# Optimization experiments

Measured on AMD Instinct MI355X. Metric: run time of the kernel, lower is better.

## Reference

```python
import jax, jax.numpy as jnp
import numpy as np

B, C, HD, NL, NP = 2, 256, 8, 4, 4
D = C // HD
SHAPES = np.array([[128, 128], [64, 64], [32, 32], [16, 16]], dtype=np.int64)
LV = int(SHAPES.prod(axis=1).sum())  # 21760
LQ = LV


def _bilinear(v_l, loc, Hl, Wl):
    # v_l: [B, HD, Nl, D]; loc: [B, Q, HD, P, 2] normalized to [0,1]
    # Matches torch grid_sample(bilinear, padding='zeros', align_corners=False)
    Bq, Q, _, P, _ = loc.shape
    x = loc[..., 0] * Wl - 0.5
    y = loc[..., 1] * Hl - 0.5
    x0f = jnp.floor(x)
    y0f = jnp.floor(y)
    lx, ly = x - x0f, y - y0f
    x0 = x0f.astype(jnp.int32)
    y0 = y0f.astype(jnp.int32)

    def corner(xi, yi, w):
        valid = (xi >= 0) & (xi < Wl) & (yi >= 0) & (yi < Hl)
        idx = jnp.clip(yi, 0, Hl - 1) * Wl + jnp.clip(xi, 0, Wl - 1)  # [B,Q,HD,P]
        idx = idx.transpose(0, 2, 1, 3).reshape(Bq, HD, Q * P)
        g = jnp.take_along_axis(v_l, idx[..., None], axis=2).reshape(Bq, HD, Q, P, D)
        wm = jnp.where(valid, w, 0.0).transpose(0, 2, 1, 3)[..., None]  # [B,HD,Q,P,1]
        return g * wm

    return (corner(x0, y0, (1 - lx) * (1 - ly))
            + corner(x0 + 1, y0, lx * (1 - ly))
            + corner(x0, y0 + 1, (1 - lx) * ly)
            + corner(x0 + 1, y0 + 1, lx * ly))


def _msda(query, reference_points, value, shapes, W_off, b_off, W_attn, b_attn, W_val, b_val, W_out, b_out):
    # value projection -> per-head layout [B, HD, Lv, D]
    v = (value @ W_val + b_val).reshape(B, LV, HD, D).transpose(0, 2, 1, 3)
    off = (query @ W_off + b_off).reshape(B, LQ, HD, NL, NP, 2)
    aw = jax.nn.softmax((query @ W_attn + b_attn).reshape(B, LQ, HD, NL * NP), axis=-1)
    aw = aw.reshape(B, LQ, HD, NL, NP)
    norm = jnp.asarray(shapes[:, ::-1].copy(), query.dtype)  # (W_l, H_l) per level
    # sampling locations: [B, Lq, HD, NL, NP, 2]
    loc = reference_points[:, :, None, :, None, :] + off / norm[None, None, None, :, None, :]
    out = jnp.zeros((B, HD, LQ, D), query.dtype)
    start = 0
    for l in range(NL):  # small static loop over feature levels
        Hl, Wl = int(shapes[l, 0]), int(shapes[l, 1])
        samp = _bilinear(v[:, :, start:start + Hl * Wl], loc[:, :, :, l], Hl, Wl)  # [B,HD,Q,P,D]
        out = out + jnp.einsum('bhqpd,bhqp->bhqd', samp, aw[:, :, :, l].transpose(0, 2, 1, 3))
        start += Hl * Wl
    out = out.transpose(0, 2, 1, 3).reshape(B, LQ, C)
    # output projection + residual (identity = query, dropout inactive at eval)
    return out @ W_out + b_out + query


def setup_inputs():
    key = jax.random.key(0)
    ks = jax.random.split(key, 8)
    sc = 1.0 / np.sqrt(C)
    return {
        "query": jax.random.normal(ks[0], (B, LQ, C), jnp.float32),
        "reference_points": jax.random.uniform(ks[1], (B, LQ, NL, 2), dtype=jnp.float32),
        "value": jax.random.normal(ks[2], (B, LV, C), jnp.float32),
        "spatial_shapes": SHAPES,
        "level_start_index": np.concatenate([[0], np.cumsum(SHAPES.prod(axis=1))[:-1]]).astype(np.int64),
        "W_off": jax.random.normal(ks[3], (C, HD * NL * NP * 2), jnp.float32) * 0.01,
        "b_off": jax.random.normal(ks[4], (HD * NL * NP * 2,), jnp.float32) * 0.01,
        "W_attn": jax.random.normal(ks[5], (C, HD * NL * NP), jnp.float32) * 0.02,
        "b_attn": jnp.zeros((HD * NL * NP,), jnp.float32),
        "W_val": jax.random.normal(ks[6], (C, C), jnp.float32) * sc,
        "b_val": jnp.zeros((C,), jnp.float32),
        "W_out": jax.random.normal(ks[7], (C, C), jnp.float32) * sc,
        "b_out": jnp.zeros((C,), jnp.float32),
    }


def reference(query, reference_points, value, spatial_shapes, level_start_index, W_off, b_off, W_attn, b_attn, W_val, b_val, W_out, b_out):
    shapes = np.asarray(spatial_shapes)  # static level geometry
    del level_start_index  # level offsets derived directly from shapes
    return _msda(query, reference_points, value, shapes, W_off, b_off, W_attn, b_attn, W_val, b_val, W_out, b_out)
```

## Files before the change

### kernel.cpp

```cpp
#include <hip/hip_runtime.h>

#define LQN 21760
#define LVN 21760
#define BATCH 2
#define CDIM 256
#define HDN 8
#define DDIM 32
#define PADCELLS 22736

typedef __attribute__((ext_vector_type(8))) short short8;
typedef __attribute__((ext_vector_type(4))) float f32x4;
typedef __attribute__((ext_vector_type(2))) float f32x2;

__device__ __forceinline__ unsigned short f2bf(float f) {
  union { float f; unsigned int u; } v; v.f = f;
  unsigned int r = v.u + 0x7fffu + ((v.u >> 16) & 1u);
  return (unsigned short)(r >> 16);
}
__device__ __forceinline__ float bflo(unsigned int u) {
  union { unsigned int u; float f; } v; v.u = u << 16; return v.f;
}
__device__ __forceinline__ float bfhi(unsigned int u) {
  union { unsigned int u; float f; } v; v.u = u & 0xffff0000u; return v.f;
}
__device__ __forceinline__ unsigned pk2bf(float lo, float hi) {
  unsigned r;
  asm("v_cvt_pk_bf16_f32 %0, %1, %2" : "=v"(r) : "v"(lo), "v"(hi));
  return r;
}

template <int IMM>
__device__ __forceinline__ float swzf(float v) {
  return __int_as_float(__builtin_amdgcn_ds_swizzle(__float_as_int(v), IMM));
}
template <int IMM>
__device__ __forceinline__ unsigned swzu(unsigned v) {
  return (unsigned)__builtin_amdgcn_ds_swizzle((int)v, IMM);
}

__global__ __launch_bounds__(256) void zero_border_kernel(
    unsigned short* __restrict__ vbf) {
  const int img = blockIdx.y;
  const int tid = blockIdx.x * 256 + threadIdx.x;
  const int cell = tid >> 2;
  const int chunk = tid & 3;
  if (cell >= 976) return;
  const int lvl = (cell >= 516) + (cell >= 776) + (cell >= 908);
  const int base = (lvl == 0) ? 0 : (lvl == 1) ? 516 : (lvl == 2) ? 776 : 908;
  const int W2 = (lvl == 0) ? 130 : (lvl == 1) ? 66 : (lvl == 2) ? 34 : 18;
  const int pst = (lvl == 0) ? 0 : (lvl == 1) ? 16900 : (lvl == 2) ? 21256 : 22412;
  const int b = cell - base;
  int x, y;
  if (b < W2) { y = 0; x = b; }
  else if (b < 2 * W2) { y = W2 - 1; x = b - W2; }
  else { const int r = b - 2 * W2; y = 1 + (r >> 1); x = (r & 1) ? (W2 - 1) : 0; }
  const size_t off = (((size_t)img * PADCELLS + pst + y * W2 + x) << 5) + chunk * 8;
  *(uint4*)(vbf + off) = (uint4){0u, 0u, 0u, 0u};
}

__global__ __launch_bounds__(256) void prep_kernel(
    const float* __restrict__ Wval, const float* __restrict__ Woff,
    const float* __restrict__ Wattn, const float* __restrict__ Wout,
    unsigned short* __restrict__ wtval, unsigned short* __restrict__ wtoa,
    unsigned short* __restrict__ wtout) {
  int idx = blockIdx.x * 256 + threadIdx.x;
  int n = idx >> 8, k = idx & 255;
  if (idx < 65536) {
    wtval[idx] = f2bf(Wval[k * 256 + n]);
    wtout[idx] = f2bf(Wout[k * 256 + n]);
  }
  if (idx < 98304) {
    float v = (n < 256) ? Woff[k * 256 + n] : Wattn[k * 128 + (n - 256)];
    wtoa[idx] = f2bf(v);
  }
}

template <int MODE>
__global__ __launch_bounds__(256) void gemm_kernel(
    const float* __restrict__ Af32, const unsigned short* __restrict__ Abf,
    const unsigned short* __restrict__ Wt, const float* __restrict__ bias0,
    const float* __restrict__ bias1, const float* __restrict__ resid,
    unsigned short* __restrict__ out_bf, float* __restrict__ out_f32) {
  constexpr int K = 256;
  constexpr int LDSS = 40;
  __shared__ unsigned short lsA[2][128 * LDSS];
  __shared__ unsigned short lsB[2][128 * LDSS];
  const int m0 = blockIdx.x * 128;
  const int n0 = blockIdx.y * 128;
  const int t = threadIdx.x;
  const int w = t >> 6;
  const int l = t & 63;
  const int wr = (w >> 1) * 64;
  const int wc = (w & 1) * 64;
  const int fr = l & 15;
  const int kk = (l >> 4) * 8;

  f32x4 acc[4][4];
#pragma unroll
  for (int mi = 0; mi < 4; ++mi)
#pragma unroll
    for (int ci = 0; ci < 4; ++ci) acc[mi][ci] = (f32x4){0.f, 0.f, 0.f, 0.f};

  const int srow = t >> 1;
  const int sk = (t & 1) * 16;

  float4 fa[4];
  uint4 ua2[2];
  uint4 ub[2];

#define LOADA(kt)                                                           \
  do {                                                                      \
    const int k0_ = (kt) * 32;                                              \
    if (MODE == 2) {                                                        \
      const unsigned short* ap = Abf + (size_t)(m0 + srow) * K + k0_ + sk;  \
      ua2[0] = *(const uint4*)ap;                                           \
      ua2[1] = *(const uint4*)(ap + 8);                                     \
    } else {                                                                \
      const float* ap = Af32 + (size_t)(m0 + srow) * K + k0_ + sk;          \
      fa[0] = *(const float4*)(ap);                                         \
      fa[1] = *(const float4*)(ap + 4);                                     \
      fa[2] = *(const float4*)(ap + 8);                                     \
      fa[3] = *(const float4*)(ap + 12);                                    \
    }                                                                       \
    const unsigned short* bp = Wt + (size_t)(n0 + srow) * K + k0_ + sk;     \
    ub[0] = *(const uint4*)bp;                                              \
    ub[1] = *(const uint4*)(bp + 8);                                        \
  } while (0)

#define STOREL(buf)                                                         \
  do {                                                                      \
    unsigned short* la = &lsA[buf][0];                                      \
    unsigned short* lb = &lsB[buf][0];                                      \
    if (MODE == 2) {                                                        \
      *(uint4*)(la + srow * LDSS + sk) = ua2[0];                            \
      *(uint4*)(la + srow * LDSS + sk + 8) = ua2[1];                        \
    } else {                                                                \
      uint4 p0, p1;                                                         \
      p0.x = pk2bf(fa[0].x, fa[0].y);                                       \
      p0.y = pk2bf(fa[0].z, fa[0].w);                                       \
      p0.z = pk2bf(fa[1].x, fa[1].y);                                       \
      p0.w = pk2bf(fa[1].z, fa[1].w);                                       \
      p1.x = pk2bf(fa[2].x, fa[2].y);                                       \
      p1.y = pk2bf(fa[2].z, fa[2].w);                                       \
      p1.z = pk2bf(fa[3].x, fa[3].y);                                       \
      p1.w = pk2bf(fa[3].z, fa[3].w);                                       \
      *(uint4*)(la + srow * LDSS + sk) = p0;                                \
      *(uint4*)(la + srow * LDSS + sk + 8) = p1;                            \
    }                                                                       \
    *(uint4*)(lb + srow * LDSS + sk) = ub[0];                               \
    *(uint4*)(lb + srow * LDSS + sk + 8) = ub[1];                           \
  } while (0)

  LOADA(0);
  STOREL(0);
  __syncthreads();

#pragma unroll
  for (int kt = 0; kt < 8; ++kt) {
    if (kt < 7) LOADA(kt + 1);
    const unsigned short* la = &lsA[kt & 1][0];
    const unsigned short* lb = &lsB[kt & 1][0];
    short8 af[4], bfr[4];
#pragma unroll
    for (int mi = 0; mi < 4; ++mi)
      af[mi] = *(const short8*)(la + (wr + mi * 16 + fr) * LDSS + kk);
#pragma unroll
    for (int ci = 0; ci < 4; ++ci)
      bfr[ci] = *(const short8*)(lb + (wc + ci * 16 + fr) * LDSS + kk);
#pragma unroll
    for (int mi = 0; mi < 4; ++mi)
#pragma unroll
      for (int ci = 0; ci < 4; ++ci)
        acc[mi][ci] = __builtin_amdgcn_mfma_f32_16x16x32_bf16(
            af[mi], bfr[ci], acc[mi][ci], 0, 0, 0);
    if (kt < 7) STOREL((kt + 1) & 1);
    __syncthreads();
  }
#undef LOADA
#undef STOREL

  const int fq = l >> 4;
  if (MODE == 0) {
    int rbase[16];
#pragma unroll
    for (int mi = 0; mi < 4; ++mi) {
#pragma unroll
      for (int r = 0; r < 4; ++r) {
        const int row = m0 + wr + mi * 16 + fq * 4 + r;
        const int bb = (row >= LVN) ? 1 : 0;
        const int i = row - bb * LVN;
        const int lvl = (i >= 16384) + (i >= 20480) + (i >= 21504);
        const int stl = (lvl == 0) ? 0 : (lvl == 1) ? 16384 : (lvl == 2) ? 20480 : 21504;
        const int pst = (lvl == 0) ? 0 : (lvl == 1) ? 16900 : (lvl == 2) ? 21256 : 22412;
        const int lw = 7 - lvl;
        const int Wl = 128 >> lvl;
        const int loc = i - stl;
        const int y = loc >> lw;
        const int x = loc & (Wl - 1);
        const int pidx = pst + (y + 1) * (Wl + 2) + (x + 1);
        rbase[mi * 4 + r] = bb * (HDN * PADCELLS * DDIM) + pidx * DDIM;
      }
    }
#pragma unroll
    for (int ci = 0; ci < 4; ++ci) {
      const int col = n0 + wc + ci * 16 + fr;
      const float bias = bias0[col];
      const int cterm = (col >> 5) * (PADCELLS * DDIM) + (col & 31);
#pragma unroll
      for (int mi = 0; mi < 4; ++mi) {
#pragma unroll
        for (int r = 0; r < 4; r += 2) {
          const unsigned u =
              pk2bf(acc[mi][ci][r] + bias, acc[mi][ci][r + 1] + bias);
          out_bf[(size_t)(rbase[mi * 4 + r] + cterm)] = (unsigned short)u;
          out_bf[(size_t)(rbase[mi * 4 + r + 1] + cterm)] =
              (unsigned short)(u >> 16);
        }
      }
    }
  } else if (MODE == 1) {
#pragma unroll
    for (int ci = 0; ci < 4; ++ci) {
      const int col = n0 + wc + ci * 16 + fr;
      const float bias = (col < 256) ? bias0[col] : bias1[col - 256];
#pragma unroll
      for (int mi = 0; mi < 4; ++mi) {
        const int row0 = m0 + wr + mi * 16 + fq * 4;
#pragma unroll
        for (int r = 0; r < 4; r += 2) {
          const unsigned u =
              pk2bf(acc[mi][ci][r] + bias, acc[mi][ci][r + 1] + bias);
          out_bf[(size_t)(row0 + r) * 384 + col] = (unsigned short)u;
          out_bf[(size_t)(row0 + r + 1) * 384 + col] = (unsigned short)(u >> 16);
        }
      }
    }
  } else {
#pragma unroll
    for (int ci = 0; ci < 4; ++ci) {
      const int col = n0 + wc + ci * 16 + fr;
      const float bias = bias0[col];
#pragma unroll
      for (int mi = 0; mi < 4; ++mi) {
#pragma unroll
        for (int r = 0; r < 4; ++r) {
          const int row = m0 + wr + mi * 16 + fq * 4 + r;
          const size_t o = (size_t)row * 256 + col;
          out_f32[o] = acc[mi][ci][r] + bias + resid[o];
        }
      }
    }
  }
}

__global__ __launch_bounds__(256) void sampler_kernel(
    const unsigned short* __restrict__ vbf,
    const unsigned short* __restrict__ offattn,
    const float* __restrict__ refpts,
    unsigned short* __restrict__ msout) {
  const int lid = blockIdx.x;
  const int pair = lid & 7;
  const int k = lid >> 3;
  const int img = pair * 2 + (k & 1);
  const int qchunk = k >> 1;
  const int h = img & 7;
  const int bb = img >> 3;

  const int t = threadIdx.x;
  const int lane = t & 63;
  const int qloc = qchunk * 64 + (t >> 6) * 16 + (lane >> 2);
  const int qi = bb * LQN + qloc;
  const int j = lane & 3;
  const int d0 = j * 8;

  const unsigned short* oa = offattn + (size_t)qi * 384;

  const int Wl = 128 >> j;
  const int W2 = Wl + 2;
  const int pst = (j == 0) ? 0 : (j == 1) ? 16900 : (j == 2) ? 21256 : 22412;
  const float fw = (float)Wl;

  const uint2 lr = *(const uint2*)(oa + 256 + h * 16 + j * 4);
  const float l0 = bflo(lr.x), l1 = bfhi(lr.x);
  const float l2 = bflo(lr.y), l3 = bfhi(lr.y);
  float mx = fmaxf(fmaxf(l0, l1), fmaxf(l2, l3));
  mx = fmaxf(mx, swzf<0x041F>(mx));
  mx = fmaxf(mx, swzf<0x081F>(mx));
  const float e0v = __expf(l0 - mx), e1v = __expf(l1 - mx);
  const float e2v = __expf(l2 - mx), e3v = __expf(l3 - mx);
  float s = (e0v + e1v) + (e2v + e3v);
  s += swzf<0x041F>(s);
  s += swzf<0x081F>(s);
  const float inv = 1.f / s;
  const float aw4[4] = {e0v * inv, e1v * inv, e2v * inv, e3v * inv};

  const float2 rf = *(const float2*)(refpts + (size_t)qi * 8 + j * 2);
  const uint4 ov = *(const uint4*)(oa + h * 32 + j * 8);
  const unsigned op_[4] = {ov.x, ov.y, ov.z, ov.w};

  unsigned eo[4][4];
  float wt[4][4];
#pragma unroll
  for (int pt = 0; pt < 4; ++pt) {
    const float ox = bflo(op_[pt]);
    const float oy = bfhi(op_[pt]);
    const float xs = fmaf(rf.x, fw, ox) - 0.5f;
    const float ys = fmaf(rf.y, fw, oy) - 0.5f;
    const float x0f = floorf(xs), y0f = floorf(ys);
    const float lx = xs - x0f, ly = ys - y0f;
    const int x0 = (int)x0f, y0 = (int)y0f;
    const float a = aw4[pt];
    const float wy1 = a * ly, wy0 = a - wy1;
    const float w01v = wy0 * lx, w00v = wy0 - w01v;
    const float w11v = wy1 * lx, w10v = wy1 - w11v;
    const int xb0 = min(max(x0 + 1, 0), Wl + 1);
    const int xb1 = min(max(x0 + 2, 0), Wl + 1);
    const int yb0 = min(max(y0 + 1, 0), Wl + 1);
    const int yb1 = min(max(y0 + 2, 0), Wl + 1);
    const unsigned r0 = (unsigned)(pst + yb0 * W2);
    const unsigned r1 = (unsigned)(pst + yb1 * W2);
    eo[pt][0] = (r0 + xb0) << 5;
    eo[pt][1] = (r0 + xb1) << 5;
    eo[pt][2] = (r1 + xb0) << 5;
    eo[pt][3] = (r1 + xb1) << 5;
    wt[pt][0] = w00v; wt[pt][1] = w01v; wt[pt][2] = w10v; wt[pt][3] = w11v;
  }

  const unsigned headbase =
      (unsigned)img * (PADCELLS * DDIM) + (unsigned)d0;

  f32x2 acc0 = (f32x2){0.f, 0.f}, acc1 = (f32x2){0.f, 0.f};
  f32x2 acc2 = (f32x2){0.f, 0.f}, acc3 = (f32x2){0.f, 0.f};

#define ACCUM(rv, wgt)                                 \
  {                                                    \
    f32x2 v_;                                          \
    v_.x = bflo(rv.x); v_.y = bfhi(rv.x);              \
    acc0 += v_ * (wgt);                                \
    v_.x = bflo(rv.y); v_.y = bfhi(rv.y);              \
    acc1 += v_ * (wgt);                                \
    v_.x = bflo(rv.z); v_.y = bfhi(rv.z);              \
    acc2 += v_ * (wgt);                                \
    v_.x = bflo(rv.w); v_.y = bfhi(rv.w);              \
    acc3 += v_ * (wgt);                                \
  }

#define POINT(LVL, PT)                                                  \
  {                                                                     \
    constexpr int IMM = (LVL << 5) | 0x1C;                              \
    const unsigned o00 = swzu<IMM>(eo[PT][0]);                          \
    const unsigned o01 = swzu<IMM>(eo[PT][1]);                          \
    const unsigned o10 = swzu<IMM>(eo[PT][2]);                          \
    const unsigned o11 = swzu<IMM>(eo[PT][3]);                          \
    const float w00 = swzf<IMM>(wt[PT][0]);                             \
    const float w01 = swzf<IMM>(wt[PT][1]);                             \
    const float w10 = swzf<IMM>(wt[PT][2]);                             \
    const float w11 = swzf<IMM>(wt[PT][3]);                             \
    const uint4 v00 = *(const uint4*)(vbf + headbase + o00);            \
    const uint4 v01 = *(const uint4*)(vbf + headbase + o01);            \
    const uint4 v10 = *(const uint4*)(vbf + headbase + o10);            \
    const uint4 v11 = *(const uint4*)(vbf + headbase + o11);            \
    ACCUM(v00, w00)                                                     \
    ACCUM(v01, w01)                                                     \
    ACCUM(v10, w10)                                                     \
    ACCUM(v11, w11)                                                     \
  }

  POINT(0, 0) POINT(0, 1) POINT(0, 2) POINT(0, 3)
  POINT(1, 0) POINT(1, 1) POINT(1, 2) POINT(1, 3)
  POINT(2, 0) POINT(2, 1) POINT(2, 2) POINT(2, 3)
  POINT(3, 0) POINT(3, 1) POINT(3, 2) POINT(3, 3)
#undef POINT
#undef ACCUM

  uint4 outv;
  outv.x = pk2bf(acc0.x, acc0.y);
  outv.y = pk2bf(acc1.x, acc1.y);
  outv.z = pk2bf(acc2.x, acc2.y);
  outv.w = pk2bf(acc3.x, acc3.y);
  *(uint4*)(msout + (size_t)qi * 256 + h * 32 + d0) = outv;
}

extern "C" void kernel_launch(void* const* d_in, const int* in_sizes, int n_in,
                              void* d_out, int out_size, void* d_ws,
                              size_t ws_size, hipStream_t stream) {
  const float* query = (const float*)d_in[0];
  const float* refpts = (const float*)d_in[1];
  const float* value = (const float*)d_in[2];
  const float* W_off = (const float*)d_in[5];
  const float* b_off = (const float*)d_in[6];
  const float* W_attn = (const float*)d_in[7];
  const float* b_attn = (const float*)d_in[8];
  const float* W_val = (const float*)d_in[9];
  const float* b_val = (const float*)d_in[10];
  const float* W_out = (const float*)d_in[11];
  const float* b_out = (const float*)d_in[12];
  float* out = (float*)d_out;

  char* ws = (char*)d_ws;
  unsigned short* wtval = (unsigned short*)(ws);
  unsigned short* wtoa = (unsigned short*)(ws + 131072);
  unsigned short* wtout = (unsigned short*)(ws + 327680);
  unsigned short* vbf = (unsigned short*)(ws + 458752);
  unsigned short* offattn = (unsigned short*)(ws + 23740416);
  unsigned short* msout = (unsigned short*)(ws + 57163776);

  zero_border_kernel<<<dim3(16, 16), 256, 0, stream>>>(vbf);
  prep_kernel<<<384, 256, 0, stream>>>(W_val, W_off, W_attn, W_out, wtval, wtoa,
                                       wtout);
  gemm_kernel<0><<<dim3(340, 2), 256, 0, stream>>>(
      value, nullptr, wtval, b_val, nullptr, nullptr, vbf, nullptr);
  gemm_kernel<1><<<dim3(340, 3), 256, 0, stream>>>(
      query, nullptr, wtoa, b_off, b_attn, nullptr, offattn, nullptr);
  sampler_kernel<<<5440, 256, 0, stream>>>(vbf, offattn, refpts, msout);
  gemm_kernel<2><<<dim3(340, 2), 256, 0, stream>>>(
      nullptr, msout, wtout, b_out, nullptr, query, nullptr, out);
}
```

Baseline: 176.2 us.

## Merge prep/zero kernels and value/offset GEMMs into fewer launches, coalesce GEMM loads

Folds the border-zeroing kernel into the weight-prep kernel and runs the value and offset/attention projection GEMMs as one interleaved 1700-block launch, cutting two launches and letting both GEMMs share the GPU. The GEMM tile loaders now have consecutive threads read consecutive 16-byte chunks across more rows instead of two wide chunks per row, which is meant to improve global-load coalescing and LDS store patterns. The merged GEMM kernel has a runtime branch on block ID, which may add some register pressure.

```diff
diff --git a/kernel.cpp b/kernel.cpp
--- a/kernel.cpp
+++ b/kernel.cpp
@@ -38,55 +38,54 @@
   return (unsigned)__builtin_amdgcn_ds_swizzle((int)v, IMM);
 }
 
-__global__ __launch_bounds__(256) void zero_border_kernel(
-    unsigned short* __restrict__ vbf) {
-  const int img = blockIdx.y;
-  const int tid = blockIdx.x * 256 + threadIdx.x;
-  const int cell = tid >> 2;
-  const int chunk = tid & 3;
-  if (cell >= 976) return;
-  const int lvl = (cell >= 516) + (cell >= 776) + (cell >= 908);
-  const int base = (lvl == 0) ? 0 : (lvl == 1) ? 516 : (lvl == 2) ? 776 : 908;
-  const int W2 = (lvl == 0) ? 130 : (lvl == 1) ? 66 : (lvl == 2) ? 34 : 18;
-  const int pst = (lvl == 0) ? 0 : (lvl == 1) ? 16900 : (lvl == 2) ? 21256 : 22412;
-  const int b = cell - base;
-  int x, y;
-  if (b < W2) { y = 0; x = b; }
-  else if (b < 2 * W2) { y = W2 - 1; x = b - W2; }
-  else { const int r = b - 2 * W2; y = 1 + (r >> 1); x = (r & 1) ? (W2 - 1) : 0; }
-  const size_t off = (((size_t)img * PADCELLS + pst + y * W2 + x) << 5) + chunk * 8;
-  *(uint4*)(vbf + off) = (uint4){0u, 0u, 0u, 0u};
-}
-
-__global__ __launch_bounds__(256) void prep_kernel(
+__global__ __launch_bounds__(256) void prep_zero_kernel(
     const float* __restrict__ Wval, const float* __restrict__ Woff,
     const float* __restrict__ Wattn, const float* __restrict__ Wout,
     unsigned short* __restrict__ wtval, unsigned short* __restrict__ wtoa,
-    unsigned short* __restrict__ wtout) {
-  int idx = blockIdx.x * 256 + threadIdx.x;
-  int n = idx >> 8, k = idx & 255;
-  if (idx < 65536) {
-    wtval[idx] = f2bf(Wval[k * 256 + n]);
-    wtout[idx] = f2bf(Wout[k * 256 + n]);
-  }
-  if (idx < 98304) {
-    float v = (n < 256) ? Woff[k * 256 + n] : Wattn[k * 128 + (n - 256)];
+    unsigned short* __restrict__ wtout, unsigned short* __restrict__ vbf) {
+  const int b = blockIdx.x;
+  if (b < 384) {
+    const int idx = b * 256 + threadIdx.x;
+    const int n = idx >> 8, k = idx & 255;
+    if (idx < 65536) {
+      wtval[idx] = f2bf(Wval[k * 256 + n]);
+      wtout[idx] = f2bf(Wout[k * 256 + n]);
+    }
+    const float v = (n < 256) ? Woff[k * 256 + n] : Wattn[k * 128 + (n - 256)];
     wtoa[idx] = f2bf(v);
+  } else {
+    const int b2 = b - 384;
+    const int img = b2 >> 4;
+    const int tid = (b2 & 15) * 256 + threadIdx.x;
+    const int cell = tid >> 2;
+    const int chunk = tid & 3;
+    if (cell >= 976) return;
+    const int lvl = (cell >= 516) + (cell >= 776) + (cell >= 908);
+    const int base = (lvl == 0) ? 0 : (lvl == 1) ? 516 : (lvl == 2) ? 776 : 908;
+    const int W2 = (lvl == 0) ? 130 : (lvl == 1) ? 66 : (lvl == 2) ? 34 : 18;
+    const int pst = (lvl == 0) ? 0 : (lvl == 1) ? 16900 : (lvl == 2) ? 21256 : 22412;
+    const int bb = cell - base;
+    int x, y;
+    if (bb < W2) { y = 0; x = bb; }
+    else if (bb < 2 * W2) { y = W2 - 1; x = bb - W2; }
+    else { const int r = bb - 2 * W2; y = 1 + (r >> 1); x = (r & 1) ? (W2 - 1) : 0; }
+    const size_t off = (((size_t)img * PADCELLS + pst + y * W2 + x) << 5) + chunk * 8;
+    *(uint4*)(vbf + off) = (uint4){0u, 0u, 0u, 0u};
   }
 }
 
 template <int MODE>
-__global__ __launch_bounds__(256) void gemm_kernel(
+__device__ __forceinline__ void gemm_body(
+    unsigned short* lsA0, unsigned short* lsB0, const int bx, const int by,
     const float* __restrict__ Af32, const unsigned short* __restrict__ Abf,
     const unsigned short* __restrict__ Wt, const float* __restrict__ bias0,
     const float* __restrict__ bias1, const float* __restrict__ resid,
     unsigned short* __restrict__ out_bf, float* __restrict__ out_f32) {
   constexpr int K = 256;
   constexpr int LDSS = 40;
-  __shared__ unsigned short lsA[2][128 * LDSS];
-  __shared__ unsigned short lsB[2][128 * LDSS];
-  const int m0 = blockIdx.x * 128;
-  const int n0 = blockIdx.y * 128;
+  constexpr int LBUF = 128 * LDSS;
+  const int m0 = bx * 128;
+  const int n0 = by * 128;
   const int t = threadIdx.x;
   const int w = t >> 6;
   const int l = t & 63;
@@ -101,54 +100,49 @@
 #pragma unroll
     for (int ci = 0; ci < 4; ++ci) acc[mi][ci] = (f32x4){0.f, 0.f, 0.f, 0.f};
 
-  const int srow = t >> 1;
-  const int sk = (t & 1) * 16;
+  const int ar8 = t >> 3, ak8 = (t & 7) * 4;
+  const int ar4 = t >> 2, ak4 = (t & 3) * 8;
 
   float4 fa[4];
   uint4 ua2[2];
   uint4 ub[2];
 
-#define LOADA(kt)                                                           \
-  do {                                                                      \
-    const int k0_ = (kt) * 32;                                              \
-    if (MODE == 2) {                                                        \
-      const unsigned short* ap = Abf + (size_t)(m0 + srow) * K + k0_ + sk;  \
-      ua2[0] = *(const uint4*)ap;                                           \
-      ua2[1] = *(const uint4*)(ap + 8);                                     \
-    } else {                                                                \
-      const float* ap = Af32 + (size_t)(m0 + srow) * K + k0_ + sk;          \
-      fa[0] = *(const float4*)(ap);                                         \
-      fa[1] = *(const float4*)(ap + 4);                                     \
-      fa[2] = *(const float4*)(ap + 8);                                     \
-      fa[3] = *(const float4*)(ap + 12);                                    \
-    }                                                                       \
-    const unsigned short* bp = Wt + (size_t)(n0 + srow) * K + k0_ + sk;     \
-    ub[0] = *(const uint4*)bp;                                              \
-    ub[1] = *(const uint4*)(bp + 8);                                        \
+#define LOADA(kt)                                                            \
+  do {                                                                       \
+    const int k0_ = (kt) * 32;                                               \
+    if (MODE == 2) {                                                         \
+      ua2[0] = *(const uint4*)(Abf + (size_t)(m0 + ar4) * K + k0_ + ak4);    \
+      ua2[1] = *(const uint4*)(Abf + (size_t)(m0 + 64 + ar4) * K + k0_ + ak4);\
+    } else {                                                                 \
+      fa[0] = *(const float4*)(Af32 + (size_t)(m0 + ar8) * K + k0_ + ak8);   \
+      fa[1] = *(const float4*)(Af32 + (size_t)(m0 + 32 + ar8) * K + k0_ + ak8);\
+      fa[2] = *(const float4*)(Af32 + (size_t)(m0 + 64 + ar8) * K + k0_ + ak8);\
+      fa[3] = *(const float4*)(Af32 + (size_t)(m0 + 96 + ar8) * K + k0_ + ak8);\
+    }                                                                        \
+    ub[0] = *(const uint4*)(Wt + (size_t)(n0 + ar4) * K + k0_ + ak4);        \
+    ub[1] = *(const uint4*)(Wt + (size_t)(n0 + 64 + ar4) * K + k0_ + ak4);   \
   } while (0)
 
-#define STOREL(buf)                                                         \
-  do {                                                                      \
-    unsigned short* la = &lsA[buf][0];                                      \
-    unsigned short* lb = &lsB[buf][0];                                      \
-    if (MODE == 2) {                                                        \
-      *(uint4*)(la + srow * LDSS + sk) = ua2[0];                            \
-      *(uint4*)(la + srow * LDSS + sk + 8) = ua2[1];                        \
-    } else {                                                                \
-      uint4 p0, p1;                                                         \
-      p0.x = pk2bf(fa[0].x, fa[0].y);                                       \
-      p0.y = pk2bf(fa[0].z, fa[0].w);                                       \
-      p0.z = pk2bf(fa[1].x, fa[1].y);                                       \
-      p0.w = pk2bf(fa[1].z, fa[1].w);                                       \
-      p1.x = pk2bf(fa[2].x, fa[2].y);                                       \
-      p1.y = pk2bf(fa[2].z, fa[2].w);                                       \
-      p1.z = pk2bf(fa[3].x, fa[3].y);                                       \
-      p1.w = pk2bf(fa[3].z, fa[3].w);                                       \
-      *(uint4*)(la + srow * LDSS + sk) = p0;                                \
-      *(uint4*)(la + srow * LDSS + sk + 8) = p1;                            \
-    }                                                                       \
-    *(uint4*)(lb + srow * LDSS + sk) = ub[0];                               \
-    *(uint4*)(lb + srow * LDSS + sk + 8) = ub[1];                           \
+#define STOREL(buf)                                                          \
+  do {                                                                       \
+    unsigned short* la = lsA0 + (buf)*LBUF;                                  \
+    unsigned short* lb = lsB0 + (buf)*LBUF;                                  \
+    if (MODE == 2) {                                                         \
+      *(uint4*)(la + ar4 * LDSS + ak4) = ua2[0];                             \
+      *(uint4*)(la + (64 + ar4) * LDSS + ak4) = ua2[1];                      \
+    } else {                                                                 \
+      uint2 q;                                                               \
+      q.x = pk2bf(fa[0].x, fa[0].y); q.y = pk2bf(fa[0].z, fa[0].w);          \
+      *(uint2*)(la + ar8 * LDSS + ak8) = q;                                  \
+      q.x = pk2bf(fa[1].x, fa[1].y); q.y = pk2bf(fa[1].z, fa[1].w);          \
+      *(uint2*)(la + (32 + ar8) * LDSS + ak8) = q;                           \
+      q.x = pk2bf(fa[2].x, fa[2].y); q.y = pk2bf(fa[2].z, fa[2].w);          \
+      *(uint2*)(la + (64 + ar8) * LDSS + ak8) = q;                           \
+      q.x = pk2bf(fa[3].x, fa[3].y); q.y = pk2bf(fa[3].z, fa[3].w);          \
+      *(uint2*)(la + (96 + ar8) * LDSS + ak8) = q;                           \
+    }                                                                        \
+    *(uint4*)(lb + ar4 * LDSS + ak4) = ub[0];                                \
+    *(uint4*)(lb + (64 + ar4) * LDSS + ak4) = ub[1];                         \
   } while (0)
 
   LOADA(0);
@@ -158,8 +152,8 @@
 #pragma unroll
   for (int kt = 0; kt < 8; ++kt) {
     if (kt < 7) LOADA(kt + 1);
-    const unsigned short* la = &lsA[kt & 1][0];
-    const unsigned short* lb = &lsB[kt & 1][0];
+    const unsigned short* la = lsA0 + (kt & 1) * LBUF;
+    const unsigned short* lb = lsB0 + (kt & 1) * LBUF;
     short8 af[4], bfr[4];
 #pragma unroll
     for (int mi = 0; mi < 4; ++mi)
@@ -251,6 +245,35 @@
       }
     }
   }
+}
+
+__global__ __launch_bounds__(256) void gemm01_kernel(
+    const float* __restrict__ value, const float* __restrict__ query,
+    const unsigned short* __restrict__ wtval,
+    const unsigned short* __restrict__ wtoa, const float* __restrict__ b_val,
+    const float* __restrict__ b_off, const float* __restrict__ b_attn,
+    unsigned short* __restrict__ vbf, unsigned short* __restrict__ offattn) {
+  __shared__ unsigned short lsA[2 * 128 * 40];
+  __shared__ unsigned short lsB[2 * 128 * 40];
+  const int bid = blockIdx.x;
+  const int g = bid % 5, u = bid / 5;
+  if (g < 2) {
+    gemm_body<0>(lsA, lsB, u, g, value, nullptr, wtval, b_val, nullptr,
+                 nullptr, vbf, nullptr);
+  } else {
+    gemm_body<1>(lsA, lsB, u, g - 2, query, nullptr, wtoa, b_off, b_attn,
+                 nullptr, offattn, nullptr);
+  }
+}
+
+__global__ __launch_bounds__(256) void gemm2_kernel(
+    const unsigned short* __restrict__ msout,
+    const unsigned short* __restrict__ wtout, const float* __restrict__ b_out,
+    const float* __restrict__ query, float* __restrict__ out) {
+  __shared__ unsigned short lsA[2 * 128 * 40];
+  __shared__ unsigned short lsB[2 * 128 * 40];
+  gemm_body<2>(lsA, lsB, blockIdx.x, blockIdx.y, nullptr, msout, wtout, b_out,
+               nullptr, query, nullptr, out);
 }
 
 __global__ __launch_bounds__(256) void sampler_kernel(
@@ -405,14 +428,11 @@
   unsigned short* offattn = (unsigned short*)(ws + 23740416);
   unsigned short* msout = (unsigned short*)(ws + 57163776);
 
-  zero_border_kernel<<<dim3(16, 16), 256, 0, stream>>>(vbf);
-  prep_kernel<<<384, 256, 0, stream>>>(W_val, W_off, W_attn, W_out, wtval, wtoa,
-                                       wtout);
-  gemm_kernel<0><<<dim3(340, 2), 256, 0, stream>>>(
-      value, nullptr, wtval, b_val, nullptr, nullptr, vbf, nullptr);
-  gemm_kernel<1><<<dim3(340, 3), 256, 0, stream>>>(
-      query, nullptr, wtoa, b_off, b_attn, nullptr, offattn, nullptr);
+  prep_zero_kernel<<<640, 256, 0, stream>>>(W_val, W_off, W_attn, W_out, wtval,
+                                            wtoa, wtout, vbf);
+  gemm01_kernel<<<1700, 256, 0, stream>>>(value, query, wtval, wtoa, b_val,
+                                          b_off, b_attn, vbf, offattn);
   sampler_kernel<<<5440, 256, 0, stream>>>(vbf, offattn, refpts, msout);
-  gemm_kernel<2><<<dim3(340, 2), 256, 0, stream>>>(
-      nullptr, msout, wtout, b_out, nullptr, query, nullptr, out);
-}
+  gemm2_kernel<<<dim3(340, 2), 256, 0, stream>>>(msout, wtout, b_out, query,
+                                                 out);
+}
```

After: 165.4 us. -6.1%, faster.
